# Kernel tuning notes

Measured on AMD Instinct MI355X. Metric: run time of the kernel, lower is better.

Reference implementation:

```python
import jax, jax.numpy as jnp
import numpy as np

HIDDEN = 896
SPLIT = HIDDEN // 2  # 448
QUANT = 256
BATCH = 8192


def _linear_init(key, out_dim, in_dim):
    # torch nn.Linear default init: U(-1/sqrt(in), 1/sqrt(in))
    bound = 1.0 / np.sqrt(in_dim)
    return jax.random.uniform(key, (out_dim, in_dim), minval=-bound, maxval=bound, dtype=jnp.float32)


def setup_inputs() -> dict:
    key = jax.random.key(0)
    ks = jax.random.split(key, 16)
    inp = {
        "prev_y": jax.random.uniform(ks[0], (BATCH, 2), dtype=jnp.float32),
        "prev_hidden": jax.random.normal(ks[1], (BATCH, HIDDEN), dtype=jnp.float32),
        "current_coarse": jax.random.uniform(ks[2], (BATCH, 1), dtype=jnp.float32),
        # recurrent projections (no bias)
        "W_Ru": _linear_init(ks[3], HIDDEN, HIDDEN),
        "W_Rr": _linear_init(ks[4], HIDDEN, HIDDEN),
        "W_Re": _linear_init(ks[5], HIDDEN, HIDDEN),
        # input projections (no bias)
        "W_Ic": _linear_init(ks[6], 3 * SPLIT, 2),
        "W_If": _linear_init(ks[7], 3 * SPLIT, 3),
        # output MLPs (with bias)
        "W_O1": _linear_init(ks[8], SPLIT, SPLIT),
        "b_O1": jnp.zeros((SPLIT,), jnp.float32),
        "W_O2": _linear_init(ks[9], QUANT, SPLIT),
        "b_O2": jnp.zeros((QUANT,), jnp.float32),
        "W_O3": _linear_init(ks[10], SPLIT, SPLIT),
        "b_O3": jnp.zeros((SPLIT,), jnp.float32),
        "W_O4": _linear_init(ks[11], QUANT, SPLIT),
        "b_O4": jnp.zeros((QUANT,), jnp.float32),
        # gate biases
        "bias_u": jnp.zeros((HIDDEN,), jnp.float32),
        "bias_r": jnp.zeros((HIDDEN,), jnp.float32),
        "bias_e": jnp.zeros((HIDDEN,), jnp.float32),
    }
    return inp


def reference(prev_y, prev_hidden, current_coarse,
              W_Ru, W_Rr, W_Re, W_Ic, W_If,
              W_O1, b_O1, W_O2, b_O2, W_O3, b_O3, W_O4, b_O4,
              bias_u, bias_r, bias_e):
    # recurrent projections: [B, H]
    R_u = prev_hidden @ W_Ru.T
    R_r = prev_hidden @ W_Rr.T
    R_e = prev_hidden @ W_Re.T

    # coarse input projection: [B, 3*SPLIT] -> three [B, SPLIT]
    cproj = prev_y @ W_Ic.T
    Ic_u, Ic_r, Ic_e = jnp.split(cproj, 3, axis=1)

    # fine input projection from [prev_y, current_coarse]: [B, 3]
    fine_in = jnp.concatenate([prev_y, current_coarse], axis=1)
    fproj = fine_in @ W_If.T
    If_u, If_r, If_e = jnp.split(fproj, 3, axis=1)

    I_u = jnp.concatenate([Ic_u, If_u], axis=1)  # [B, H]
    I_r = jnp.concatenate([Ic_r, If_r], axis=1)
    I_e = jnp.concatenate([Ic_e, If_e], axis=1)

    u = jax.nn.sigmoid(R_u + I_u + bias_u)
    r = jax.nn.sigmoid(R_r + I_r + bias_r)
    e = jnp.tanh(r * R_e + I_e + bias_e)
    hidden = u * prev_hidden + (1.0 - u) * e  # [B, H]

    h_c, h_f = jnp.split(hidden, 2, axis=1)  # each [B, SPLIT]
    out_coarse = jax.nn.relu(h_c @ W_O1.T + b_O1) @ W_O2.T + b_O2  # [B, QUANT]
    out_fine = jax.nn.relu(h_f @ W_O3.T + b_O3) @ W_O4.T + b_O4    # [B, QUANT]
    return (out_coarse, out_fine, hidden)
```

## Files before the change

### kernel.cpp

```cpp
#include <hip/hip_runtime.h>
#include <hip/hip_bf16.h>

typedef __hip_bfloat16 bf16;
typedef __attribute__((ext_vector_type(8))) short short8;
typedef __attribute__((ext_vector_type(4))) float f32x4;

#define AS1 __attribute__((address_space(1)))
#define AS3 __attribute__((address_space(3)))

__device__ __forceinline__ void gld_lds16(const bf16* g, bf16* l) {
    __builtin_amdgcn_global_load_lds((const AS1 void*)g, (AS3 void*)l, 16, 0, 0);
}


__global__ __launch_bounds__(256)
void k_convert(const float* __restrict__ s0,
               const float* __restrict__ s1,
               const float* __restrict__ s2,
               const float* __restrict__ s3,
               const float* __restrict__ s4,
               const float* __restrict__ s5,
               const float* __restrict__ s6,
               const float* __restrict__ s7,
               bf16* __restrict__ dst)
{
    const size_t B0 =  7340032, B1 =  8142848, B2 =  8945664, B3 = 9748480,
                 B4 =  9949184, B5 = 10063872, B6 = 10264576;
    size_t t = ((size_t)blockIdx.x * 256 + threadIdx.x) * 8;
    const float* s; size_t off;
    if      (t < B0) { s = s0; off = t; }
    else if (t < B1) { s = s1; off = t - B0; }
    else if (t < B2) { s = s2; off = t - B1; }
    else if (t < B3) { s = s3; off = t - B2; }
    else if (t < B4) { s = s4; off = t - B3; }
    else if (t < B5) { s = s5; off = t - B4; }
    else if (t < B6) { s = s6; off = t - B5; }
    else             { s = s7; off = t - B6; }
    float4 a = *(const float4*)(s + off);
    float4 b = *(const float4*)(s + off + 4);
    union { short8 v; bf16 h[8]; } u;
    u.h[0] = (bf16)a.x; u.h[1] = (bf16)a.y; u.h[2] = (bf16)a.z; u.h[3] = (bf16)a.w;
    u.h[4] = (bf16)b.x; u.h[5] = (bf16)b.y; u.h[6] = (bf16)b.z; u.h[7] = (bf16)b.w;
    *(short8*)(dst + t) = u.v;
}

__global__ __launch_bounds__(256, 2)
void k_gates(const float* __restrict__ prev_y,
             const bf16*  __restrict__ prev_hb,
             const float* __restrict__ prev_hf,
             const float* __restrict__ cc,
             const bf16*  __restrict__ Wu,
             const bf16*  __restrict__ Wr,
             const bf16*  __restrict__ We,
             const float* __restrict__ Wic,
             const float* __restrict__ Wif,
             const float* __restrict__ bu_,
             const float* __restrict__ br_,
             const float* __restrict__ be_,
             float* __restrict__ hidden_f,
             bf16*  __restrict__ hidden_b)
{
    __shared__ bf16 At[128 * 64];
    __shared__ bf16 Bt[3][64 * 64];

    const int tid  = threadIdx.x;
    const int wid  = tid >> 6;
    const int lane = tid & 63;
    const int quad = lane >> 4;
    const int l16  = lane & 15;
    const int sw   = l16 & 7;
    const int wm   = (wid >> 1) * 64;
    const int wn   = (wid & 1) * 32;
    const int bm   = blockIdx.x;
    const int bn   = blockIdx.y;
    const int srow = tid >> 3;
    const int sp   = tid & 7;
    const int scol = sp * 8;
    const int gcol = ((sp ^ (srow & 7)) * 8);

    const bf16* Wg[3] = {Wu, Wr, We};

    f32x4 acc[3][4][2] = {};

    const size_t a_base = (size_t)(bm * 128) * 896;
    const size_t b_base = (size_t)(bn * 64) * 896;

    for (int k0 = 0; k0 < 896; k0 += 64) {
        __syncthreads();
#pragma unroll
        for (int i = 0; i < 4; ++i) {
            int r = i * 32 + srow;
            gld_lds16(prev_hb + a_base + (size_t)r * 896 + k0 + gcol,
                      &At[r * 64 + scol]);
        }
#pragma unroll
        for (int g = 0; g < 3; ++g) {
#pragma unroll
            for (int j = 0; j < 2; ++j) {
                int r = j * 32 + srow;
                gld_lds16(Wg[g] + b_base + (size_t)r * 896 + k0 + gcol,
                          &Bt[g][r * 64 + scol]);
            }
        }
        __syncthreads();

#pragma unroll
        for (int ks = 0; ks < 2; ++ks) {
            const int pk = ((ks * 4 + quad) ^ sw) * 8;
            short8 af[4];
#pragma unroll
            for (int m = 0; m < 4; ++m)
                af[m] = *(const short8*)&At[(wm + m * 16 + l16) * 64 + pk];
#pragma unroll
            for (int g = 0; g < 3; ++g) {
#pragma unroll
                for (int n = 0; n < 2; ++n) {
                    short8 bfr = *(const short8*)&Bt[g][(wn + n * 16 + l16) * 64 + pk];
#pragma unroll
                    for (int m = 0; m < 4; ++m)
                        acc[g][m][n] = __builtin_amdgcn_mfma_f32_16x16x32_bf16(
                            af[m], bfr, acc[g][m][n], 0, 0, 0);
                }
            }
        }
    }

    float wu_[2][3], wr2[2][3], we2[2][3], bu[2], br[2], be[2];
    int hcol[2];
#pragma unroll
    for (int n = 0; n < 2; ++n) {
        int h = bn * 64 + wn + n * 16 + l16;
        hcol[n] = h;
        bu[n] = bu_[h];
        br[n] = br_[h];
        be[n] = be_[h];
        if (h < 448) {
            wu_[n][0] = Wic[h * 2];           wu_[n][1] = Wic[h * 2 + 1];           wu_[n][2] = 0.f;
            wr2[n][0] = Wic[(h + 448) * 2];   wr2[n][1] = Wic[(h + 448) * 2 + 1];   wr2[n][2] = 0.f;
            we2[n][0] = Wic[(h + 896) * 2];   we2[n][1] = Wic[(h + 896) * 2 + 1];   we2[n][2] = 0.f;
        } else {
            int hf = h - 448;
            wu_[n][0] = Wif[hf * 3];           wu_[n][1] = Wif[hf * 3 + 1];           wu_[n][2] = Wif[hf * 3 + 2];
            wr2[n][0] = Wif[(hf + 448) * 3];   wr2[n][1] = Wif[(hf + 448) * 3 + 1];   wr2[n][2] = Wif[(hf + 448) * 3 + 2];
            we2[n][0] = Wif[(hf + 896) * 3];   we2[n][1] = Wif[(hf + 896) * 3 + 1];   we2[n][2] = Wif[(hf + 896) * 3 + 2];
        }
    }
#pragma unroll
    for (int m = 0; m < 4; ++m) {
#pragma unroll
        for (int i = 0; i < 4; ++i) {
            int b = bm * 128 + wm + m * 16 + quad * 4 + i;
            float py0 = prev_y[b * 2];
            float py1 = prev_y[b * 2 + 1];
            float c   = cc[b];
#pragma unroll
            for (int n = 0; n < 2; ++n) {
                float Iu = py0 * wu_[n][0] + py1 * wu_[n][1] + c * wu_[n][2];
                float Ir = py0 * wr2[n][0] + py1 * wr2[n][1] + c * wr2[n][2];
                float Ie = py0 * we2[n][0] + py1 * we2[n][1] + c * we2[n][2];
                float u = 1.f / (1.f + __expf(-(acc[0][m][n][i] + Iu + bu[n])));
                float r = 1.f / (1.f + __expf(-(acc[1][m][n][i] + Ir + br[n])));
                float x = r * acc[2][m][n][i] + Ie + be[n];
                float ex = __expf(2.f * x);
                float e = 1.f - 2.f / (ex + 1.f);
                size_t idx = (size_t)b * 896 + hcol[n];
                float ph = prev_hf[idx];
                float hv = u * ph + (1.f - u) * e;
                hidden_f[idx] = hv;
                hidden_b[idx] = (bf16)hv;
            }
        }
    }
}

__global__ __launch_bounds__(256, 4)
void k_gemm_bt2(const bf16* __restrict__ A0, const bf16* __restrict__ A1, int a_stride,
                const bf16* __restrict__ B0, const bf16* __restrict__ B1,
                const float* __restrict__ bias0, const float* __restrict__ bias1,
                bf16* __restrict__ Cb0, bf16* __restrict__ Cb1,
                float* __restrict__ Cf0, float* __restrict__ Cf1,
                int c_stride, int K, int relu)
{
    __shared__ bf16 At[128 * 64];
    __shared__ bf16 Bt[64 * 64];

    const int z = blockIdx.z;
    const bf16*  A    = z ? A1 : A0;
    const bf16*  B    = z ? B1 : B0;
    const float* bias = z ? bias1 : bias0;
    bf16*  Cb = z ? Cb1 : Cb0;
    float* Cf = z ? Cf1 : Cf0;

    const int tid  = threadIdx.x;
    const int wid  = tid >> 6;
    const int lane = tid & 63;
    const int quad = lane >> 4;
    const int l16  = lane & 15;
    const int sw   = l16 & 7;
    const int wm   = (wid >> 1) * 64;
    const int wn   = (wid & 1) * 32;
    const int bm   = blockIdx.x;
    const int bn   = blockIdx.y;
    const int srow = tid >> 3;
    const int sp   = tid & 7;
    const int scol = sp * 8;
    const int gcol = ((sp ^ (srow & 7)) * 8);

    f32x4 acc[4][2] = {};

    const size_t a_base = (size_t)(bm * 128) * a_stride;
    const size_t b_base = (size_t)(bn * 64) * K;

    for (int k0 = 0; k0 < K; k0 += 64) {
        __syncthreads();
#pragma unroll
        for (int i = 0; i < 4; ++i) {
            int r = i * 32 + srow;
            gld_lds16(A + a_base + (size_t)r * a_stride + k0 + gcol,
                      &At[r * 64 + scol]);
        }
#pragma unroll
        for (int j = 0; j < 2; ++j) {
            int r = j * 32 + srow;
            gld_lds16(B + b_base + (size_t)r * K + k0 + gcol,
                      &Bt[r * 64 + scol]);
        }
        __syncthreads();

#pragma unroll
        for (int ks = 0; ks < 2; ++ks) {
            const int pk = ((ks * 4 + quad) ^ sw) * 8;
            short8 af[4];
#pragma unroll
            for (int m = 0; m < 4; ++m)
                af[m] = *(const short8*)&At[(wm + m * 16 + l16) * 64 + pk];
#pragma unroll
            for (int n = 0; n < 2; ++n) {
                short8 bfr = *(const short8*)&Bt[(wn + n * 16 + l16) * 64 + pk];
#pragma unroll
                for (int m = 0; m < 4; ++m)
                    acc[m][n] = __builtin_amdgcn_mfma_f32_16x16x32_bf16(
                        af[m], bfr, acc[m][n], 0, 0, 0);
            }
        }
    }

#pragma unroll
    for (int n = 0; n < 2; ++n) {
        int h = bn * 64 + wn + n * 16 + l16;
        float bv = bias[h];
#pragma unroll
        for (int m = 0; m < 4; ++m) {
#pragma unroll
            for (int i = 0; i < 4; ++i) {
                int row = bm * 128 + wm + m * 16 + quad * 4 + i;
                float v = acc[m][n][i] + bv;
                if (relu) v = fmaxf(v, 0.f);
                if (Cf) Cf[(size_t)row * c_stride + h] = v;
                else    Cb[(size_t)row * c_stride + h] = (bf16)v;
            }
        }
    }
}

extern "C" void kernel_launch(void* const* d_in, const int* in_sizes, int n_in,
                              void* d_out, int out_size, void* d_ws, size_t ws_size,
                              hipStream_t stream) {
    const float* prev_y = (const float*)d_in[0];
    const float* prev_h = (const float*)d_in[1];
    const float* cc     = (const float*)d_in[2];
    const float* Wu     = (const float*)d_in[3];
    const float* Wr     = (const float*)d_in[4];
    const float* We     = (const float*)d_in[5];
    const float* Wic    = (const float*)d_in[6];
    const float* Wif    = (const float*)d_in[7];
    const float* W_O1   = (const float*)d_in[8];
    const float* b_O1   = (const float*)d_in[9];
    const float* W_O2   = (const float*)d_in[10];
    const float* b_O2   = (const float*)d_in[11];
    const float* W_O3   = (const float*)d_in[12];
    const float* b_O3   = (const float*)d_in[13];
    const float* W_O4   = (const float*)d_in[14];
    const float* b_O4   = (const float*)d_in[15];
    const float* bias_u = (const float*)d_in[16];
    const float* bias_r = (const float*)d_in[17];
    const float* bias_e = (const float*)d_in[18];

    float* out      = (float*)d_out;
    float* out_c    = out;
    float* out_f    = out + (size_t)8192 * 256;
    float* hidden_f = out + (size_t)8192 * 512;

    bf16* ws       = (bf16*)d_ws;
    bf16* prev_h_b = ws;
    bf16* Wu_b     = ws + 7340032;
    bf16* Wr_b     = ws + 8142848;
    bf16* We_b     = ws + 8945664;
    bf16* W_O1_b   = ws + 9748480;
    bf16* W_O2_b   = ws + 9949184;
    bf16* W_O3_b   = ws + 10063872;
    bf16* W_O4_b   = ws + 10264576;
    bf16* hidden_b = ws + 10379264;
    bf16* inter_c  = prev_h_b;
    bf16* inter_f  = prev_h_b + 3670016;

    dim3 blk(256);

    k_convert<<<dim3(5068), blk, 0, stream>>>(prev_h, Wu, Wr, We,
                                              W_O1, W_O2, W_O3, W_O4, ws);

    k_gates<<<dim3(64, 14), blk, 0, stream>>>(prev_y, prev_h_b, prev_h, cc,
                                              Wu_b, Wr_b, We_b,
                                              Wic, Wif, bias_u, bias_r, bias_e,
                                              hidden_f, hidden_b);

    k_gemm_bt2<<<dim3(64, 7, 2), blk, 0, stream>>>(
        hidden_b, hidden_b + 448, 896,
        W_O1_b, W_O3_b, b_O1, b_O3,
        inter_c, inter_f, nullptr, nullptr, 448, 448, 1);

    k_gemm_bt2<<<dim3(64, 4, 2), blk, 0, stream>>>(
        inter_c, inter_f, 448,
        W_O2_b, W_O4_b, b_O2, b_O4,
        nullptr, nullptr, out_c, out_f, 256, 448, 0);
}
```

Measured before the change: 206.7 us.

## Fuse two output MLP GEMMs into one kernel with LDS-resident intermediate

Replaces the two separate output-head GEMM launches with a single kernel. Each block keeps a 64-row slice of the hidden state in LDS, computes the ReLU intermediate into LDS, then runs the second GEMM directly from it. Weight tiles are streamed through a four-deep LDS ring, two k-steps per barrier. This removes the global round-trip of the bf16 intermediate and one launch. The cost is about 144KB of LDS per block, which allows only one block per CU, and a grid of just 256 blocks, so occupancy and latency hiding are reduced.

```diff
diff --git a/kernel.cpp b/kernel.cpp
--- a/kernel.cpp
+++ b/kernel.cpp
@@ -173,23 +173,24 @@
     }
 }
 
-__global__ __launch_bounds__(256, 4)
-void k_gemm_bt2(const bf16* __restrict__ A0, const bf16* __restrict__ A1, int a_stride,
-                const bf16* __restrict__ B0, const bf16* __restrict__ B1,
-                const float* __restrict__ bias0, const float* __restrict__ bias1,
-                bf16* __restrict__ Cb0, bf16* __restrict__ Cb1,
-                float* __restrict__ Cf0, float* __restrict__ Cf1,
-                int c_stride, int K, int relu)
+__global__ __launch_bounds__(256)
+void k_heads(const bf16* __restrict__ hb,
+             const bf16* __restrict__ W1c, const bf16* __restrict__ W1f,
+             const bf16* __restrict__ W2c, const bf16* __restrict__ W2f,
+             const float* __restrict__ b1c, const float* __restrict__ b1f,
+             const float* __restrict__ b2c, const float* __restrict__ b2f,
+             float* __restrict__ outc, float* __restrict__ outf)
 {
-    __shared__ bf16 At[128 * 64];
-    __shared__ bf16 Bt[64 * 64];
-
-    const int z = blockIdx.z;
-    const bf16*  A    = z ? A1 : A0;
-    const bf16*  B    = z ? B1 : B0;
-    const float* bias = z ? bias1 : bias0;
-    bf16*  Cb = z ? Cb1 : Cb0;
-    float* Cf = z ? Cf1 : Cf0;
+    __shared__ bf16 Ah[64 * 448];
+    __shared__ bf16 Ih[64 * 448];
+    __shared__ bf16 Wt[4][64 * 64];
+
+    const int z = blockIdx.y;
+    const bf16*  W1 = z ? W1f : W1c;
+    const bf16*  W2 = z ? W2f : W2c;
+    const float* b1 = z ? b1f : b1c;
+    const float* b2 = z ? b2f : b2c;
+    float*       op = z ? outf : outc;
 
     const int tid  = threadIdx.x;
     const int wid  = tid >> 6;
@@ -197,69 +198,122 @@
     const int quad = lane >> 4;
     const int l16  = lane & 15;
     const int sw   = l16 & 7;
-    const int wm   = (wid >> 1) * 64;
+    const int wm   = (wid >> 1) * 32;
     const int wn   = (wid & 1) * 32;
     const int bm   = blockIdx.x;
-    const int bn   = blockIdx.y;
     const int srow = tid >> 3;
     const int sp   = tid & 7;
-    const int scol = sp * 8;
-    const int gcol = ((sp ^ (srow & 7)) * 8);
-
-    f32x4 acc[4][2] = {};
-
-    const size_t a_base = (size_t)(bm * 128) * a_stride;
-    const size_t b_base = (size_t)(bn * 64) * K;
-
-    for (int k0 = 0; k0 < K; k0 += 64) {
-        __syncthreads();
-#pragma unroll
-        for (int i = 0; i < 4; ++i) {
-            int r = i * 32 + srow;
-            gld_lds16(A + a_base + (size_t)r * a_stride + k0 + gcol,
-                      &At[r * 64 + scol]);
-        }
+
+    {
+        const size_t base = (size_t)(bm * 64) * 896 + (size_t)z * 448;
+#pragma unroll
+        for (int i = 0; i < 14; ++i) {
+            int p   = i * 256 + tid;
+            int row = p / 56;
+            int pc  = p - row * 56;
+            int lc  = (pc & ~7) | ((pc ^ row) & 7);
+            gld_lds16(hb + base + (size_t)row * 896 + lc * 8, &Ah[p * 8]);
+        }
+    }
+
+    auto stageW = [&](const bf16* W, int nc, int k0, int buf) {
 #pragma unroll
         for (int j = 0; j < 2; ++j) {
             int r = j * 32 + srow;
-            gld_lds16(B + b_base + (size_t)r * K + k0 + gcol,
-                      &Bt[r * 64 + scol]);
-        }
-        __syncthreads();
-
+            gld_lds16(W + (size_t)(nc * 64 + r) * 448 + k0 + ((sp ^ (r & 7)) << 3),
+                      &Wt[buf][r * 64 + sp * 8]);
+        }
+    };
+
+    f32x4 acc[2][2] = {};
+
+    auto compute = [&](const bf16* Asrc, int k0, int buf) {
 #pragma unroll
         for (int ks = 0; ks < 2; ++ks) {
             const int pk = ((ks * 4 + quad) ^ sw) * 8;
-            short8 af[4];
-#pragma unroll
-            for (int m = 0; m < 4; ++m)
-                af[m] = *(const short8*)&At[(wm + m * 16 + l16) * 64 + pk];
-#pragma unroll
-            for (int n = 0; n < 2; ++n) {
-                short8 bfr = *(const short8*)&Bt[(wn + n * 16 + l16) * 64 + pk];
-#pragma unroll
-                for (int m = 0; m < 4; ++m)
+            short8 af[2], bfr[2];
+#pragma unroll
+            for (int m = 0; m < 2; ++m)
+                af[m] = *(const short8*)&Asrc[(wm + m * 16 + l16) * 448 + k0 + pk];
+#pragma unroll
+            for (int n = 0; n < 2; ++n)
+                bfr[n] = *(const short8*)&Wt[buf][(wn + n * 16 + l16) * 64 + pk];
+#pragma unroll
+            for (int m = 0; m < 2; ++m)
+#pragma unroll
+                for (int n = 0; n < 2; ++n)
                     acc[m][n] = __builtin_amdgcn_mfma_f32_16x16x32_bf16(
-                        af[m], bfr, acc[m][n], 0, 0, 0);
-            }
-        }
-    }
-
-#pragma unroll
-    for (int n = 0; n < 2; ++n) {
-        int h = bn * 64 + wn + n * 16 + l16;
-        float bv = bias[h];
-#pragma unroll
-        for (int m = 0; m < 4; ++m) {
-#pragma unroll
-            for (int i = 0; i < 4; ++i) {
-                int row = bm * 128 + wm + m * 16 + quad * 4 + i;
-                float v = acc[m][n][i] + bv;
-                if (relu) v = fmaxf(v, 0.f);
-                if (Cf) Cf[(size_t)row * c_stride + h] = v;
-                else    Cb[(size_t)row * c_stride + h] = (bf16)v;
-            }
-        }
+                        af[m], bfr[n], acc[m][n], 0, 0, 0);
+        }
+    };
+
+    auto epiB = [&](int nc) {
+#pragma unroll
+        for (int n = 0; n < 2; ++n) {
+            int col = nc * 64 + wn + n * 16 + l16;
+            float bv = b1[col];
+            int lcb = col >> 3, ce = col & 7;
+#pragma unroll
+            for (int m = 0; m < 2; ++m)
+#pragma unroll
+                for (int i = 0; i < 4; ++i) {
+                    int row = wm + m * 16 + quad * 4 + i;
+                    int pcb = (lcb & ~7) | ((lcb ^ row) & 7);
+                    Ih[row * 448 + pcb * 8 + ce] = (bf16)fmaxf(acc[m][n][i] + bv, 0.f);
+                }
+        }
+#pragma unroll
+        for (int m = 0; m < 2; ++m)
+#pragma unroll
+            for (int n = 0; n < 2; ++n)
+                acc[m][n] = f32x4{0.f, 0.f, 0.f, 0.f};
+    };
+
+    auto epiC = [&](int nc) {
+#pragma unroll
+        for (int n = 0; n < 2; ++n) {
+            int col = nc * 64 + wn + n * 16 + l16;
+            float bv = b2[col];
+#pragma unroll
+            for (int m = 0; m < 2; ++m)
+#pragma unroll
+                for (int i = 0; i < 4; ++i) {
+                    int row = wm + m * 16 + quad * 4 + i;
+                    op[(size_t)(bm * 64 + row) * 256 + col] = acc[m][n][i] + bv;
+                }
+        }
+#pragma unroll
+        for (int m = 0; m < 2; ++m)
+#pragma unroll
+            for (int n = 0; n < 2; ++n)
+                acc[m][n] = f32x4{0.f, 0.f, 0.f, 0.f};
+    };
+
+    stageW(W1, 0, 0, 0);
+    stageW(W1, 0, 64, 1);
+    for (int i = 0; i < 49; i += 2) {
+        __syncthreads();
+        if (i + 2 < 49) stageW(W1, (i + 2) / 7, ((i + 2) % 7) * 64, (i + 2) & 3);
+        if (i + 3 < 49) stageW(W1, (i + 3) / 7, ((i + 3) % 7) * 64, (i + 3) & 3);
+        compute(Ah, (i % 7) * 64, i & 3);
+        if (i % 7 == 6) epiB(i / 7);
+        if (i + 1 < 49) {
+            compute(Ah, ((i + 1) % 7) * 64, (i + 1) & 3);
+            if ((i + 1) % 7 == 6) epiB((i + 1) / 7);
+        }
+    }
+    __syncthreads();
+
+    stageW(W2, 0, 0, 0);
+    stageW(W2, 0, 64, 1);
+    for (int i = 0; i < 28; i += 2) {
+        __syncthreads();
+        if (i + 2 < 28) stageW(W2, (i + 2) / 7, ((i + 2) % 7) * 64, (i + 2) & 3);
+        if (i + 3 < 28) stageW(W2, (i + 3) / 7, ((i + 3) % 7) * 64, (i + 3) & 3);
+        compute(Ih, (i % 7) * 64, i & 3);
+        if (i % 7 == 6) epiC(i / 7);
+        compute(Ih, ((i + 1) % 7) * 64, (i + 1) & 3);
+        if ((i + 1) % 7 == 6) epiC((i + 1) / 7);
     }
 }
 
@@ -301,8 +355,6 @@
     bf16* W_O3_b   = ws + 10063872;
     bf16* W_O4_b   = ws + 10264576;
     bf16* hidden_b = ws + 10379264;
-    bf16* inter_c  = prev_h_b;
-    bf16* inter_f  = prev_h_b + 3670016;
 
     dim3 blk(256);
 
@@ -314,13 +366,8 @@
                                               Wic, Wif, bias_u, bias_r, bias_e,
                                               hidden_f, hidden_b);
 
-    k_gemm_bt2<<<dim3(64, 7, 2), blk, 0, stream>>>(
-        hidden_b, hidden_b + 448, 896,
-        W_O1_b, W_O3_b, b_O1, b_O3,
-        inter_c, inter_f, nullptr, nullptr, 448, 448, 1);
-
-    k_gemm_bt2<<<dim3(64, 4, 2), blk, 0, stream>>>(
-        inter_c, inter_f, 448,
-        W_O2_b, W_O4_b, b_O2, b_O4,
-        nullptr, nullptr, out_c, out_f, 256, 448, 0);
-}
+    k_heads<<<dim3(128, 2), blk, 0, stream>>>(hidden_b,
+                                              W_O1_b, W_O3_b, W_O2_b, W_O4_b,
+                                              b_O1, b_O3, b_O2, b_O4,
+                                              out_c, out_f);
+}
```

New measurement: 226.0 us. 1.09x slower.
